# Optimization experiments

Hardware: AMD Instinct MI355X
Metric: run time of the kernel (lower is better)

## Reference

```python
import jax, jax.numpy as jnp
import numpy as np

EPS = 1e-5
WBIT = 4
ABIT = 4

def _ste_round(x):
    return x + jax.lax.stop_gradient(jnp.round(x) - x)

def quantize_k(x, k):
    # uniform quantization to 2^k - 1 levels in [0,1], straight-through round
    n = float(2 ** k - 1)
    return _ste_round(x * n) / n

def weight_quant(w, k=WBIT):
    # DoReFa weight quantization (percentile=1.0 -> plain max)
    t = jnp.tanh(w)
    m = jnp.max(jnp.abs(t))
    wn = t / (2.0 * m) + 0.5            # in [0,1]
    return 2.0 * quantize_k(wn, k) - 1.0  # in [-1,1]

def act_quant(x, k=ABIT):
    return quantize_k(jnp.clip(x, 0.0, 1.0), k)

def bn(x, g, b, m, v):
    # inference batchnorm, per-channel (NCHW)
    scale = g / jnp.sqrt(v + EPS)
    return x * scale[None, :, None, None] + (b - m * scale)[None, :, None, None]

def conv(x, w, stride=1, pad=0, groups=1):
    return jax.lax.conv_general_dilated(
        x, w, window_strides=(stride, stride), padding=[(pad, pad), (pad, pad)],
        feature_group_count=groups, dimension_numbers=('NCHW', 'OIHW', 'NCHW'))

def setup_inputs() -> dict:
    key = jax.random.key(0)
    ks = jax.random.split(key, 17)
    N, Cin, H, W = 32, 64, 56, 56
    hidden = Cin * 6  # 384
    Cout = 64
    d = {
        'x':  jax.random.normal(ks[0], (N, Cin, H, W), jnp.float32),
        'w1': jax.random.normal(ks[1], (hidden, Cin, 1, 1), jnp.float32) * 0.1,
        'w2': jax.random.normal(ks[2], (hidden, 1, 3, 3), jnp.float32) * 0.1,
        'w3': jax.random.normal(ks[3], (Cout, hidden, 1, 1), jnp.float32) * 0.1,
        'g1': jax.random.uniform(ks[4], (hidden,), jnp.float32, 0.5, 1.5),
        'b1': jax.random.normal(ks[5], (hidden,), jnp.float32) * 0.1,
        'm1': jax.random.normal(ks[6], (hidden,), jnp.float32) * 0.1,
        'v1': jax.random.uniform(ks[7], (hidden,), jnp.float32, 0.5, 1.5),
        'g2': jax.random.uniform(ks[8], (hidden,), jnp.float32, 0.5, 1.5),
        'b2': jax.random.normal(ks[9], (hidden,), jnp.float32) * 0.1,
        'm2': jax.random.normal(ks[10], (hidden,), jnp.float32) * 0.1,
        'v2': jax.random.uniform(ks[11], (hidden,), jnp.float32, 0.5, 1.5),
        'g3': jax.random.uniform(ks[12], (Cout,), jnp.float32, 0.5, 1.5),
        'b3': jax.random.normal(ks[13], (Cout,), jnp.float32) * 0.1,
        'm3': jax.random.normal(ks[14], (Cout,), jnp.float32) * 0.1,
        'v3': jax.random.uniform(ks[15], (Cout,), jnp.float32, 0.5, 1.5),
    }
    return d

def reference(x, w1, w2, w3, g1, b1, m1, v1, g2, b2, m2, v2, g3, b3, m3, v3):
    hidden = w1.shape[0]
    shortcut = x
    h = act_quant(jax.nn.relu(bn(conv(x, weight_quant(w1)), g1, b1, m1, v1)))
    h = act_quant(jax.nn.relu(bn(conv(h, weight_quant(w2), stride=1, pad=1, groups=hidden), g2, b2, m2, v2)))
    h = act_quant(bn(conv(h, weight_quant(w3)), g3, b3, m3, v3))
    return h + shortcut  # stride==1 and in_planes==out_planes -> residual
```

## Files before the change

kernel.cpp:

```cpp
#include <hip/hip_runtime.h>
#include <hip/hip_bf16.h>

#define EPS 1e-5f
#define INV15 (1.0f/15.0f)

#define NB 32
#define CIN 64
#define HID 384
#define HH 56
#define HW 3136
#define NPIX 100352
#define BLKPB 1605632
#define NPIXU4 401408

#define OFF_BLOB1 0
#define OFF_W2T  52224
#define OFF_B2F  66048
#define OFF_BLOB3 67584
#define OFF_MAX  92672
#define OFF_H1 1048576
#define OFF_H2 20316160

typedef int v4i __attribute__((ext_vector_type(4)));
typedef float f32x4 __attribute__((ext_vector_type(4)));
typedef short bf16x8 __attribute__((ext_vector_type(8)));

__device__ __forceinline__ short splitbf(float f, float& rem) {
  __hip_bfloat16 h = __float2bfloat16(f);
  rem = f - __bfloat162float(h);
  return __builtin_bit_cast(short, h);
}

__global__ __launch_bounds__(256) void prep_max(
    const float* __restrict__ w1, const float* __restrict__ w2,
    const float* __restrict__ w3, unsigned int* __restrict__ maxout) {
  int b = blockIdx.x >> 4;
  int sub = blockIdx.x & 15;
  const float* src = (b == 0) ? w1 : (b == 1) ? w2 : w3;
  int n = (b == 1) ? HID * 9 : HID * CIN;
  float m = 0.f;
  for (int i = sub * 256 + threadIdx.x; i < n; i += 4096)
    m = fmaxf(m, fabsf(tanhf(src[i])));
  #pragma unroll
  for (int off = 32; off > 0; off >>= 1)
    m = fmaxf(m, __shfl_down(m, off, 64));
  __shared__ float red[4];
  if ((threadIdx.x & 63) == 0) red[threadIdx.x >> 6] = m;
  __syncthreads();
  if (threadIdx.x == 0) {
    m = fmaxf(fmaxf(red[0], red[1]), fmaxf(red[2], red[3]));
    atomicMax(maxout + b, __float_as_uint(m));
  }
}

__global__ __launch_bounds__(256) void prep_quant(
    const float* __restrict__ w1, const float* __restrict__ w2,
    const float* __restrict__ w3,
    const float* __restrict__ g1, const float* __restrict__ b1,
    const float* __restrict__ m1, const float* __restrict__ v1,
    const float* __restrict__ g2, const float* __restrict__ b2,
    const float* __restrict__ m2, const float* __restrict__ v2,
    const float* __restrict__ g3, const float* __restrict__ b3,
    const float* __restrict__ m3, const float* __restrict__ v3,
    char* __restrict__ ws) {
  const float* maxv = (const float*)(ws + OFF_MAX);
  int idx = blockIdx.x * 256 + threadIdx.x;
  if (idx < 24576) {
    int e = idx & 7, lane = (idx >> 3) & 63, ks = (idx >> 9) & 1, mt = idx >> 10;
    int o = mt * 16 + (lane & 15);
    int k = ks * 32 + (lane >> 4) * 8 + e;
    float t = tanhf(w1[o * 64 + k]);
    int wi = 2 * (int)rintf((t / (2.f * maxv[0]) + 0.5f) * 15.f) - 15;
    float rr;
    ((short*)(ws + OFF_BLOB1))[idx] = splitbf((float)wi, rr);
  } else if (idx < 28032) {
    int jj = idx - 24576;
    int tap = jj / 384, cl = jj - tap * 384;
    int g = cl >> 3, r = cl & 7;
    int c = 32 * (g >> 2) + ((r < 4) ? ((g & 3) * 4 + r) : (16 + (g & 3) * 4 + (r - 4)));
    float s = g2[c] / sqrtf(v2[c] + EPS);
    float t = tanhf(w2[c * 9 + tap]);
    float q = 2.f * (rintf((t / (2.f * maxv[1]) + 0.5f) * 15.f) * INV15) - 1.f;
    ((float*)(ws + OFF_W2T))[jj] = q * s * INV15;
  } else if (idx < 28416) {
    int cl = idx - 28032;
    int g = cl >> 3, r = cl & 7;
    int c = 32 * (g >> 2) + ((r < 4) ? ((g & 3) * 4 + r) : (16 + (g & 3) * 4 + (r - 4)));
    float s = g2[c] / sqrtf(v2[c] + EPS);
    ((float*)(ws + OFF_B2F))[cl] = b2[c] - m2[c] * s;
  } else if (idx < 28800) {
    int o = idx - 28416;
    ((float*)(ws + OFF_BLOB1 + 49152))[o] = g1[o] / sqrtf(v1[o] + EPS);
  } else if (idx < 29184) {
    int o = idx - 28800;
    float s = g1[o] / sqrtf(v1[o] + EPS);
    ((float*)(ws + OFF_BLOB1 + 50688))[o] = 15.f * (b1[o] - m1[o] * s);
  } else if (idx < 53760) {
    int jj = idx - 29184;
    int j = jj & 7, lane = (jj >> 3) & 63, nt = (jj >> 9) & 3, ks = jj >> 11;
    int n = nt * 16 + (lane & 15);
    int quad = lane >> 4;
    int k = ks * 32 + ((j & 1) ? (16 + quad * 4 + (j >> 1)) : (quad * 4 + (j >> 1)));
    float t = tanhf(w3[n * 384 + k]);
    int wi = 2 * (int)rintf((t / (2.f * maxv[2]) + 0.5f) * 15.f) - 15;
    (ws + OFF_BLOB3)[jj] = (char)wi;
  } else if (idx < 53824) {
    int n = idx - 53760;
    float s = g3[n] / sqrtf(v3[n] + EPS);
    *(float*)(ws + OFF_BLOB3 + 24576 + n * 4) = s * (1.f / 225.f);
  } else if (idx < 53888) {
    int n = idx - 53824;
    float s = g3[n] / sqrtf(v3[n] + EPS);
    *(float*)(ws + OFF_BLOB3 + 24832 + n * 4) = b3[n] - m3[n] * s;
  }
}

__global__ __launch_bounds__(256) void k1(
    const float* __restrict__ x, const char* __restrict__ blob1,
    char* __restrict__ h1b) {
  __shared__ uint4 sBuf[3264];
  int tid = threadIdx.x;
  {
    const uint4* src = (const uint4*)blob1;
    for (int i = tid; i < 3264; i += 256) sBuf[i] = src[i];
  }
  __syncthreads();
  const bf16x8* wf = (const bf16x8*)sBuf;
  const float* sSB = (const float*)(sBuf + 3072);

  int wv = tid >> 6, lane = tid & 63;
  int quad = lane >> 4, m = lane & 15;
  size_t pixabs = (size_t)blockIdx.x * 64 + wv * 16 + m;
  int img = blockIdx.x / 49;
  int prem = (blockIdx.x - img * 49) * 64 + wv * 16 + m;
  const float* xb = x + (size_t)img * (CIN * HW) + prem;

  bf16x8 xh[2], xl[2], xq[2];
  #pragma unroll
  for (int ks = 0; ks < 2; ks++) {
    #pragma unroll
    for (int e = 0; e < 8; e++) {
      float f = xb[(size_t)(ks * 32 + quad * 8 + e) * HW];
      float r1, r2, r3;
      xh[ks][e] = splitbf(f, r1);
      xl[ks][e] = splitbf(r1, r2);
      xq[ks][e] = splitbf(r2, r3);
    }
  }

  #pragma unroll
  for (int half = 0; half < 2; half++) {
    f32x4 acc[12];
    #pragma unroll
    for (int i = 0; i < 12; i++) { f32x4 z = {0.f, 0.f, 0.f, 0.f}; acc[i] = z; }
    #pragma unroll
    for (int i = 0; i < 12; i++) {
      int mt = half * 12 + i;
      bf16x8 w0 = wf[(mt * 2 + 0) * 64 + lane];
      bf16x8 w1 = wf[(mt * 2 + 1) * 64 + lane];
      acc[i] = __builtin_amdgcn_mfma_f32_16x16x32_bf16(w0, xh[0], acc[i], 0, 0, 0);
      acc[i] = __builtin_amdgcn_mfma_f32_16x16x32_bf16(w1, xh[1], acc[i], 0, 0, 0);
      acc[i] = __builtin_amdgcn_mfma_f32_16x16x32_bf16(w0, xl[0], acc[i], 0, 0, 0);
      acc[i] = __builtin_amdgcn_mfma_f32_16x16x32_bf16(w1, xl[1], acc[i], 0, 0, 0);
      acc[i] = __builtin_amdgcn_mfma_f32_16x16x32_bf16(w0, xq[0], acc[i], 0, 0, 0);
      acc[i] = __builtin_amdgcn_mfma_f32_16x16x32_bf16(w1, xq[1], acc[i], 0, 0, 0);
    }
    #pragma unroll
    for (int l = 0; l < 6; l++) {
      int b = half * 6 + l;
      f32x4 ae = acc[2 * l], ao = acc[2 * l + 1];
      unsigned int pk = 0;
      #pragma unroll
      for (int r = 0; r < 4; r++) {
        int oe = 32 * b + quad * 4 + r;
        int oo = oe + 16;
        float fe = fminf(fmaxf(ae[r] * sSB[oe] + sSB[384 + oe], 0.f), 15.f);
        float fo = fminf(fmaxf(ao[r] * sSB[oo] + sSB[384 + oo], 0.f), 15.f);
        pk |= ((unsigned int)(int)rintf(fe)) << (8 * r);
        pk |= ((unsigned int)(int)rintf(fo)) << (8 * r + 4);
      }
      *(unsigned int*)(h1b + (size_t)b * BLKPB + pixabs * 16 + quad * 4) = pk;
    }
  }
}

__global__ __launch_bounds__(256) void k2(
    const unsigned int* __restrict__ h1q, const float* __restrict__ W2t,
    const float* __restrict__ B2f, unsigned int* __restrict__ h2q) {
  int tid = threadIdx.x;
  int g = blockIdx.y * 16 + (tid & 15);
  int img = blockIdx.x / 196;
  int trem = blockIdx.x - img * 196;
  int pixrem = trem * 16 + (tid >> 4);
  int h = pixrem / 56;
  int w = pixrem - h * 56;
  size_t base_u = (size_t)(g >> 2) * NPIXU4 + (g & 3);
  size_t pixabs = (size_t)img * HW + pixrem;

  float4 be = *(const float4*)(B2f + g * 8);
  float4 bo = *(const float4*)(B2f + g * 8 + 4);
  float aE0 = be.x, aE1 = be.y, aE2 = be.z, aE3 = be.w;
  float aO0 = bo.x, aO1 = bo.y, aO2 = bo.z, aO3 = bo.w;

  #pragma unroll
  for (int tap = 0; tap < 9; tap++) {
    const int dh = tap / 3 - 1;
    const int dw = tap % 3 - 1;
    bool valid = ((unsigned)(h + dh) < 56u) && ((unsigned)(w + dw) < 56u);
    unsigned int u = 0u;
    if (valid) u = h1q[base_u + (pixabs + dh * 56 + dw) * 4];
    unsigned int te = u & 0x0F0F0F0Fu;
    unsigned int to = (u >> 4) & 0x0F0F0F0Fu;
    float4 wE = *(const float4*)(W2t + tap * 384 + g * 8);
    float4 wO = *(const float4*)(W2t + tap * 384 + g * 8 + 4);
    aE0 += wE.x * (float)(unsigned char)(te);
    aE1 += wE.y * (float)(unsigned char)(te >> 8);
    aE2 += wE.z * (float)(unsigned char)(te >> 16);
    aE3 += wE.w * (float)(unsigned char)(te >> 24);
    aO0 += wO.x * (float)(unsigned char)(to);
    aO1 += wO.y * (float)(unsigned char)(to >> 8);
    aO2 += wO.z * (float)(unsigned char)(to >> 16);
    aO3 += wO.w * (float)(unsigned char)(to >> 24);
  }
  unsigned int pk = 0;
  {
    unsigned int q;
    q = (unsigned int)(int)rintf(fminf(fmaxf(aE0, 0.f), 1.f) * 15.f); pk |= q;
    q = (unsigned int)(int)rintf(fminf(fmaxf(aO0, 0.f), 1.f) * 15.f); pk |= q << 4;
    q = (unsigned int)(int)rintf(fminf(fmaxf(aE1, 0.f), 1.f) * 15.f); pk |= q << 8;
    q = (unsigned int)(int)rintf(fminf(fmaxf(aO1, 0.f), 1.f) * 15.f); pk |= q << 12;
    q = (unsigned int)(int)rintf(fminf(fmaxf(aE2, 0.f), 1.f) * 15.f); pk |= q << 16;
    q = (unsigned int)(int)rintf(fminf(fmaxf(aO2, 0.f), 1.f) * 15.f); pk |= q << 20;
    q = (unsigned int)(int)rintf(fminf(fmaxf(aE3, 0.f), 1.f) * 15.f); pk |= q << 24;
    q = (unsigned int)(int)rintf(fminf(fmaxf(aO3, 0.f), 1.f) * 15.f); pk |= q << 28;
  }
  h2q[base_u + pixabs * 4] = pk;
}

__global__ __launch_bounds__(256) void InvertedBottleneck_conv_Q_13709535609694_kernel(
    const unsigned int* __restrict__ h2q, const char* __restrict__ blob,
    const float* __restrict__ x, float* __restrict__ out) {
  __shared__ long lds8[3136];
  int tid = threadIdx.x;
  {
    const long* src = (const long*)blob;
    #pragma unroll
    for (int i = 0; i < 13; i++) {
      int j = tid + i * 256;
      if (j < 3136) lds8[j] = src[j];
    }
  }
  __syncthreads();

  int wv = tid >> 6;
  int lane = tid & 63;
  int m = lane & 15;
  int quad = lane >> 4;
  int pixW = blockIdx.x * 64 + wv * 16;

  const unsigned int* aptr = h2q + (size_t)(pixW + m) * 4 + quad;
  unsigned int ua[12];
  #pragma unroll
  for (int ks = 0; ks < 12; ks++) ua[ks] = aptr[(size_t)ks * NPIXU4];

  v4i acc[4];
  #pragma unroll
  for (int nt = 0; nt < 4; nt++) { v4i z = {0,0,0,0}; acc[nt] = z; }

  #pragma unroll
  for (int ks = 0; ks < 12; ks++) {
    unsigned int u = ua[ks];
    unsigned int t = u & 0x0F0F0F0Fu;
    unsigned int s = (u >> 4) & 0x0F0F0F0Fu;
    unsigned int d0 = (t & 0xFFu) | ((s & 0xFFu) << 8) | ((t & 0xFF00u) << 8) | ((s & 0xFF00u) << 16);
    unsigned int d1 = ((t >> 16) & 0xFFu) | (((s >> 16) & 0xFFu) << 8) | ((t >> 24) << 16) | ((s >> 24) << 24);
    long aF = (long)(((unsigned long)d1 << 32) | (unsigned long)d0);
    #pragma unroll
    for (int nt = 0; nt < 4; nt++) {
      long bF = lds8[(ks * 4 + nt) * 64 + lane];
      acc[nt] = __builtin_amdgcn_mfma_i32_16x16x32_i8(aF, bF, acc[nt], 0, 0, 0);
    }
  }

  const float* scl = (const float*)(lds8 + 3072);
  int img = blockIdx.x / 49;
  int prem = (blockIdx.x - img * 49) * 64 + wv * 16 + quad * 4;

  #pragma unroll
  for (int nt = 0; nt < 4; nt++) {
    int n = nt * 16 + m;
    float sc = scl[n];
    float bi = scl[64 + n];
    size_t off = ((size_t)img * CIN + n) * HW + prem;
    const float4 xv = *(const float4*)(x + off);
    float4 ov;
    float v, a;
    v = (float)acc[nt][0] * sc + bi; a = fminf(fmaxf(v, 0.f), 1.f); ov.x = rintf(a * 15.f) * INV15 + xv.x;
    v = (float)acc[nt][1] * sc + bi; a = fminf(fmaxf(v, 0.f), 1.f); ov.y = rintf(a * 15.f) * INV15 + xv.y;
    v = (float)acc[nt][2] * sc + bi; a = fminf(fmaxf(v, 0.f), 1.f); ov.z = rintf(a * 15.f) * INV15 + xv.z;
    v = (float)acc[nt][3] * sc + bi; a = fminf(fmaxf(v, 0.f), 1.f); ov.w = rintf(a * 15.f) * INV15 + xv.w;
    *(float4*)(out + off) = ov;
  }
}

extern "C" void kernel_launch(void* const* d_in, const int* in_sizes, int n_in,
                              void* d_out, int out_size, void* d_ws, size_t ws_size,
                              hipStream_t stream) {
  const float* x  = (const float*)d_in[0];
  const float* w1 = (const float*)d_in[1];
  const float* w2 = (const float*)d_in[2];
  const float* w3 = (const float*)d_in[3];
  const float* g1 = (const float*)d_in[4];
  const float* b1 = (const float*)d_in[5];
  const float* m1 = (const float*)d_in[6];
  const float* v1 = (const float*)d_in[7];
  const float* g2 = (const float*)d_in[8];
  const float* b2 = (const float*)d_in[9];
  const float* m2 = (const float*)d_in[10];
  const float* v2 = (const float*)d_in[11];
  const float* g3 = (const float*)d_in[12];
  const float* b3 = (const float*)d_in[13];
  const float* m3 = (const float*)d_in[14];
  const float* v3 = (const float*)d_in[15];

  char* ws = (char*)d_ws;
  unsigned int* maxu = (unsigned int*)(ws + OFF_MAX);
  char* h1b = ws + OFF_H1;
  char* h2b = ws + OFF_H2;
  float* outp = (float*)d_out;

  hipMemsetAsync(maxu, 0, 12, stream);
  prep_max<<<dim3(48), dim3(256), 0, stream>>>(w1, w2, w3, maxu);
  prep_quant<<<dim3(211), dim3(256), 0, stream>>>(
      w1, w2, w3, g1, b1, m1, v1, g2, b2, m2, v2, g3, b3, m3, v3, ws);
  k1<<<dim3(1568), dim3(256), 0, stream>>>(x, ws + OFF_BLOB1, h1b);
  k2<<<dim3(6272, 3), dim3(256), 0, stream>>>(
      (const unsigned int*)h1b, (const float*)(ws + OFF_W2T),
      (const float*)(ws + OFF_B2F), (unsigned int*)h2b);
  InvertedBottleneck_conv_Q_13709535609694_kernel<<<dim3(1568), dim3(256), 0, stream>>>(
      (const unsigned int*)h2b, ws + OFF_BLOB3, x, outp);
}
```

Before: 206.0 us.

## Rewrite depthwise conv with packed int16 MADs and 4-pixel register reuse

The depthwise 3x3 stage now multiplies 4-bit activations by integer weights using packed 16-bit integer multiply-adds, two channels per instruction, with BN scale and bias applied once at the end. Each thread computes four horizontally adjacent pixels and reuses a 6-wide row window, which cuts redundant global loads. Weights and BN constants are staged in LDS. The weight max is now taken over |w| before applying tanh once, relying on tanh being monotonic. This trades float FMAs for int16 accumulation, and the wider thread tiles raise register pressure.

```diff
diff --git a/kernel.cpp b/kernel.cpp
--- a/kernel.cpp
+++ b/kernel.cpp
@@ -14,10 +14,11 @@
 #define NPIXU4 401408
 
 #define OFF_BLOB1 0
-#define OFF_W2T  52224
-#define OFF_B2F  66048
-#define OFF_BLOB3 67584
-#define OFF_MAX  92672
+#define OFF_W2PK 52224
+#define OFF_A2   59136
+#define OFF_B2   60672
+#define OFF_BLOB3 62208
+#define OFF_MAX  87296
 #define OFF_H1 1048576
 #define OFF_H2 20316160
 
@@ -29,6 +30,16 @@
   __hip_bfloat16 h = __float2bfloat16(f);
   rem = f - __bfloat162float(h);
   return __builtin_bit_cast(short, h);
+}
+
+__device__ __forceinline__ int pk_mad(unsigned int w, int a, int c) {
+  int d;
+  asm("v_pk_mad_i16 %0, %1, %2, %3" : "=v"(d) : "v"(w), "v"(a), "v"(c));
+  return d;
+}
+
+__device__ __forceinline__ int ch_of(int g, int j, int h) {
+  return 32 * (g >> 2) + 4 * (g & 3) + 16 * (j & 1) + ((j >> 1) & 1) + 2 * h;
 }
 
 __global__ __launch_bounds__(256) void prep_max(
@@ -40,7 +51,7 @@
   int n = (b == 1) ? HID * 9 : HID * CIN;
   float m = 0.f;
   for (int i = sub * 256 + threadIdx.x; i < n; i += 4096)
-    m = fmaxf(m, fabsf(tanhf(src[i])));
+    m = fmaxf(m, fabsf(src[i]));
   #pragma unroll
   for (int off = 32; off > 0; off >>= 1)
     m = fmaxf(m, __shfl_down(m, off, 64));
@@ -66,50 +77,60 @@
   const float* maxv = (const float*)(ws + OFF_MAX);
   int idx = blockIdx.x * 256 + threadIdx.x;
   if (idx < 24576) {
+    float mm = tanhf(maxv[0]);
     int e = idx & 7, lane = (idx >> 3) & 63, ks = (idx >> 9) & 1, mt = idx >> 10;
     int o = mt * 16 + (lane & 15);
     int k = ks * 32 + (lane >> 4) * 8 + e;
     float t = tanhf(w1[o * 64 + k]);
-    int wi = 2 * (int)rintf((t / (2.f * maxv[0]) + 0.5f) * 15.f) - 15;
+    int wi = 2 * (int)rintf((t / (2.f * mm) + 0.5f) * 15.f) - 15;
     float rr;
     ((short*)(ws + OFF_BLOB1))[idx] = splitbf((float)wi, rr);
-  } else if (idx < 28032) {
+  } else if (idx < 26304) {
+    float mm = tanhf(maxv[1]);
     int jj = idx - 24576;
-    int tap = jj / 384, cl = jj - tap * 384;
-    int g = cl >> 3, r = cl & 7;
-    int c = 32 * (g >> 2) + ((r < 4) ? ((g & 3) * 4 + r) : (16 + (g & 3) * 4 + (r - 4)));
+    int tap = jj / 192, rem = jj - tap * 192;
+    int g = rem >> 2, j = rem & 3;
+    int clo = ch_of(g, j, 0), chi = ch_of(g, j, 1);
+    int wlo = 2 * (int)rintf((tanhf(w2[clo * 9 + tap]) / (2.f * mm) + 0.5f) * 15.f) - 15;
+    int whi = 2 * (int)rintf((tanhf(w2[chi * 9 + tap]) / (2.f * mm) + 0.5f) * 15.f) - 15;
+    ((unsigned int*)(ws + OFF_W2PK))[jj] =
+        ((unsigned int)(unsigned short)(short)wlo) |
+        (((unsigned int)(unsigned short)(short)whi) << 16);
+  } else if (idx < 26688) {
+    int ii = idx - 26304;
+    int g = ii >> 3, j = (ii >> 1) & 3, h = ii & 1;
+    int c = ch_of(g, j, h);
     float s = g2[c] / sqrtf(v2[c] + EPS);
-    float t = tanhf(w2[c * 9 + tap]);
-    float q = 2.f * (rintf((t / (2.f * maxv[1]) + 0.5f) * 15.f) * INV15) - 1.f;
-    ((float*)(ws + OFF_W2T))[jj] = q * s * INV15;
-  } else if (idx < 28416) {
-    int cl = idx - 28032;
-    int g = cl >> 3, r = cl & 7;
-    int c = 32 * (g >> 2) + ((r < 4) ? ((g & 3) * 4 + r) : (16 + (g & 3) * 4 + (r - 4)));
+    ((float*)(ws + OFF_A2))[ii] = s * (1.f / 15.f);
+  } else if (idx < 27072) {
+    int ii = idx - 26688;
+    int g = ii >> 3, j = (ii >> 1) & 3, h = ii & 1;
+    int c = ch_of(g, j, h);
     float s = g2[c] / sqrtf(v2[c] + EPS);
-    ((float*)(ws + OFF_B2F))[cl] = b2[c] - m2[c] * s;
-  } else if (idx < 28800) {
-    int o = idx - 28416;
+    ((float*)(ws + OFF_B2))[ii] = 15.f * (b2[c] - m2[c] * s) + 0.5f;
+  } else if (idx < 27456) {
+    int o = idx - 27072;
     ((float*)(ws + OFF_BLOB1 + 49152))[o] = g1[o] / sqrtf(v1[o] + EPS);
-  } else if (idx < 29184) {
-    int o = idx - 28800;
+  } else if (idx < 27840) {
+    int o = idx - 27456;
     float s = g1[o] / sqrtf(v1[o] + EPS);
     ((float*)(ws + OFF_BLOB1 + 50688))[o] = 15.f * (b1[o] - m1[o] * s);
-  } else if (idx < 53760) {
-    int jj = idx - 29184;
+  } else if (idx < 52416) {
+    float mm = tanhf(maxv[2]);
+    int jj = idx - 27840;
     int j = jj & 7, lane = (jj >> 3) & 63, nt = (jj >> 9) & 3, ks = jj >> 11;
     int n = nt * 16 + (lane & 15);
     int quad = lane >> 4;
     int k = ks * 32 + ((j & 1) ? (16 + quad * 4 + (j >> 1)) : (quad * 4 + (j >> 1)));
     float t = tanhf(w3[n * 384 + k]);
-    int wi = 2 * (int)rintf((t / (2.f * maxv[2]) + 0.5f) * 15.f) - 15;
+    int wi = 2 * (int)rintf((t / (2.f * mm) + 0.5f) * 15.f) - 15;
     (ws + OFF_BLOB3)[jj] = (char)wi;
-  } else if (idx < 53824) {
-    int n = idx - 53760;
+  } else if (idx < 52480) {
+    int n = idx - 52416;
     float s = g3[n] / sqrtf(v3[n] + EPS);
     *(float*)(ws + OFF_BLOB3 + 24576 + n * 4) = s * (1.f / 225.f);
-  } else if (idx < 53888) {
-    int n = idx - 53824;
+  } else if (idx < 52544) {
+    int n = idx - 52480;
     float s = g3[n] / sqrtf(v3[n] + EPS);
     *(float*)(ws + OFF_BLOB3 + 24832 + n * 4) = b3[n] - m3[n] * s;
   }
@@ -185,56 +206,82 @@
 }
 
 __global__ __launch_bounds__(256) void k2(
-    const unsigned int* __restrict__ h1q, const float* __restrict__ W2t,
-    const float* __restrict__ B2f, unsigned int* __restrict__ h2q) {
+    const unsigned int* __restrict__ h1q, const char* __restrict__ wsrc,
+    unsigned int* __restrict__ h2q) {
+  __shared__ unsigned int sbuf[2496];
   int tid = threadIdx.x;
+  for (int i = tid; i < 2496; i += 256) sbuf[i] = ((const unsigned int*)wsrc)[i];
+  __syncthreads();
+  const uint4* W4 = (const uint4*)sbuf;
+  const float* Af = (const float*)(sbuf + 1728);
+  const float* Bf = Af + 384;
+
   int g = blockIdx.y * 16 + (tid & 15);
-  int img = blockIdx.x / 196;
-  int trem = blockIdx.x - img * 196;
-  int pixrem = trem * 16 + (tid >> 4);
-  int h = pixrem / 56;
-  int w = pixrem - h * 56;
+  int qid = tid >> 4;
+  int img = blockIdx.x / 49;
+  int trem = blockIdx.x - img * 49;
+  int px0 = trem * 64 + qid * 4;
+  int h = px0 / 56;
+  int w0 = px0 - h * 56;
   size_t base_u = (size_t)(g >> 2) * NPIXU4 + (g & 3);
-  size_t pixabs = (size_t)img * HW + pixrem;
-
-  float4 be = *(const float4*)(B2f + g * 8);
-  float4 bo = *(const float4*)(B2f + g * 8 + 4);
-  float aE0 = be.x, aE1 = be.y, aE2 = be.z, aE3 = be.w;
-  float aO0 = bo.x, aO1 = bo.y, aO2 = bo.z, aO3 = bo.w;
-
-  #pragma unroll
-  for (int tap = 0; tap < 9; tap++) {
-    const int dh = tap / 3 - 1;
-    const int dw = tap % 3 - 1;
-    bool valid = ((unsigned)(h + dh) < 56u) && ((unsigned)(w + dw) < 56u);
-    unsigned int u = 0u;
-    if (valid) u = h1q[base_u + (pixabs + dh * 56 + dw) * 4];
-    unsigned int te = u & 0x0F0F0F0Fu;
-    unsigned int to = (u >> 4) & 0x0F0F0F0Fu;
-    float4 wE = *(const float4*)(W2t + tap * 384 + g * 8);
-    float4 wO = *(const float4*)(W2t + tap * 384 + g * 8 + 4);
-    aE0 += wE.x * (float)(unsigned char)(te);
-    aE1 += wE.y * (float)(unsigned char)(te >> 8);
-    aE2 += wE.z * (float)(unsigned char)(te >> 16);
-    aE3 += wE.w * (float)(unsigned char)(te >> 24);
-    aO0 += wO.x * (float)(unsigned char)(to);
-    aO1 += wO.y * (float)(unsigned char)(to >> 8);
-    aO2 += wO.z * (float)(unsigned char)(to >> 16);
-    aO3 += wO.w * (float)(unsigned char)(to >> 24);
-  }
-  unsigned int pk = 0;
-  {
-    unsigned int q;
-    q = (unsigned int)(int)rintf(fminf(fmaxf(aE0, 0.f), 1.f) * 15.f); pk |= q;
-    q = (unsigned int)(int)rintf(fminf(fmaxf(aO0, 0.f), 1.f) * 15.f); pk |= q << 4;
-    q = (unsigned int)(int)rintf(fminf(fmaxf(aE1, 0.f), 1.f) * 15.f); pk |= q << 8;
-    q = (unsigned int)(int)rintf(fminf(fmaxf(aO1, 0.f), 1.f) * 15.f); pk |= q << 12;
-    q = (unsigned int)(int)rintf(fminf(fmaxf(aE2, 0.f), 1.f) * 15.f); pk |= q << 16;
-    q = (unsigned int)(int)rintf(fminf(fmaxf(aO2, 0.f), 1.f) * 15.f); pk |= q << 20;
-    q = (unsigned int)(int)rintf(fminf(fmaxf(aE3, 0.f), 1.f) * 15.f); pk |= q << 24;
-    q = (unsigned int)(int)rintf(fminf(fmaxf(aO3, 0.f), 1.f) * 15.f); pk |= q << 28;
-  }
-  h2q[base_u + pixabs * 4] = pk;
+  size_t imgrow = (size_t)img * HW;
+
+  int acc[4][4];
+  #pragma unroll
+  for (int p = 0; p < 4; p++)
+    #pragma unroll
+    for (int j = 0; j < 4; j++) acc[p][j] = 0;
+
+  #pragma unroll
+  for (int dh = 0; dh < 3; dh++) {
+    int hr = h + dh - 1;
+    bool vrow = (unsigned)hr < 56u;
+    const unsigned int* rp = h1q + base_u + (imgrow + (size_t)hr * 56) * 4;
+    int P[6][4];
+    #pragma unroll
+    for (int c = 0; c < 6; c++) {
+      int wc = w0 + c - 1;
+      unsigned int u = 0;
+      if (vrow && (unsigned)wc < 56u) u = rp[(size_t)wc * 4];
+      P[c][0] = (int)(u & 0x000F000Fu);
+      P[c][1] = (int)((u >> 4) & 0x000F000Fu);
+      P[c][2] = (int)((u >> 8) & 0x000F000Fu);
+      P[c][3] = (int)((u >> 12) & 0x000F000Fu);
+    }
+    #pragma unroll
+    for (int cw = 0; cw < 3; cw++) {
+      uint4 wvv = W4[(dh * 3 + cw) * 48 + g];
+      #pragma unroll
+      for (int p = 0; p < 4; p++) {
+        acc[p][0] = pk_mad(wvv.x, P[p + cw][0], acc[p][0]);
+        acc[p][1] = pk_mad(wvv.y, P[p + cw][1], acc[p][1]);
+        acc[p][2] = pk_mad(wvv.z, P[p + cw][2], acc[p][2]);
+        acc[p][3] = pk_mad(wvv.w, P[p + cw][3], acc[p][3]);
+      }
+    }
+  }
+
+  float Ar[8], Br[8];
+  #pragma unroll
+  for (int i = 0; i < 8; i++) { Ar[i] = Af[g * 8 + i]; Br[i] = Bf[g * 8 + i]; }
+
+  #pragma unroll
+  for (int p = 0; p < 4; p++) {
+    unsigned int pk = 0;
+    #pragma unroll
+    for (int j = 0; j < 4; j++) {
+      int a = acc[p][j];
+      int lo = (a << 16) >> 16;
+      int hi = a >> 16;
+      float vl = fmaf((float)lo, Ar[2 * j], Br[2 * j]);
+      float vh = fmaf((float)hi, Ar[2 * j + 1], Br[2 * j + 1]);
+      unsigned int ql = (unsigned int)fmaxf(fminf(vl, 15.49f), 0.f);
+      unsigned int qh = (unsigned int)fmaxf(fminf(vh, 15.49f), 0.f);
+      pk |= ql << (4 * j);
+      pk |= qh << (4 * j + 16);
+    }
+    h2q[base_u + (imgrow + (size_t)px0 + p) * 4] = pk;
+  }
 }
 
 __global__ __launch_bounds__(256) void InvertedBottleneck_conv_Q_13709535609694_kernel(
@@ -331,12 +378,11 @@
 
   hipMemsetAsync(maxu, 0, 12, stream);
   prep_max<<<dim3(48), dim3(256), 0, stream>>>(w1, w2, w3, maxu);
-  prep_quant<<<dim3(211), dim3(256), 0, stream>>>(
+  prep_quant<<<dim3(206), dim3(256), 0, stream>>>(
       w1, w2, w3, g1, b1, m1, v1, g2, b2, m2, v2, g3, b3, m3, v3, ws);
   k1<<<dim3(1568), dim3(256), 0, stream>>>(x, ws + OFF_BLOB1, h1b);
-  k2<<<dim3(6272, 3), dim3(256), 0, stream>>>(
-      (const unsigned int*)h1b, (const float*)(ws + OFF_W2T),
-      (const float*)(ws + OFF_B2F), (unsigned int*)h2b);
+  k2<<<dim3(1568, 3), dim3(256), 0, stream>>>(
+      (const unsigned int*)h1b, ws + OFF_W2PK, (unsigned int*)h2b);
   InvertedBottleneck_conv_Q_13709535609694_kernel<<<dim3(1568), dim3(256), 0, stream>>>(
       (const unsigned int*)h2b, ws + OFF_BLOB3, x, outp);
 }
```

After: 170.2 us. 1.21x faster.
